# Performance work log

Measured on AMD Instinct MI355X. Metric: run time of the kernel, lower is better.

## Reference

```python
import jax, jax.numpy as jnp
import numpy as np

B, L, IN_DIM, OUT_DIM = 8, 128, 512, 512
DEP_NUM, DEP_DIM = 45, 16


def setup_inputs() -> dict:
    key = jax.random.key(0)
    ks = jax.random.split(key, 10)
    h = jax.random.normal(ks[0], (B, L, IN_DIM), dtype=jnp.float32)
    dep_type_matrix = jax.random.randint(ks[1], (B, L, L), 0, DEP_NUM, dtype=jnp.int32)
    aspect_mask = jnp.zeros((B, L), dtype=bool).at[:, 10:14].set(True)
    # params (torch Linear convention: y = x @ W.T + b); xavier-ish scale
    def xavier(k, shape):
        fan_in, fan_out = shape[1], shape[0]
        lim = jnp.sqrt(6.0 / (fan_in + fan_out))
        return jax.random.uniform(k, shape, jnp.float32, -lim, lim)
    emb = jax.random.normal(ks[2], (DEP_NUM, DEP_DIM), dtype=jnp.float32)
    W1 = xavier(ks[3], (OUT_DIM, IN_DIM + DEP_DIM))
    b1 = jnp.zeros((OUT_DIM,), jnp.float32)
    W2 = xavier(ks[4], (OUT_DIM, IN_DIM + DEP_DIM))
    b2 = jnp.zeros((OUT_DIM,), jnp.float32)
    Wg = xavier(ks[5], (OUT_DIM, IN_DIM))
    bg = jnp.zeros((OUT_DIM,), jnp.float32)
    bias = jnp.zeros((OUT_DIM,), jnp.float32)
    return {"h": h, "dep_type_matrix": dep_type_matrix, "aspect_mask": aspect_mask,
            "emb": emb, "W1": W1, "b1": b1, "W2": W2, "b2": b2,
            "Wg": Wg, "bg": bg, "bias": bias}


def _position_aware(h, aspect_mask):
    # h: [B,L,D], aspect_mask: [B,L] bool
    Lh = h.shape[1]
    m = aspect_mask.astype(jnp.int32)
    start = jnp.argmax(m, axis=1)                       # first True
    end = Lh - 1 - jnp.argmax(jnp.flip(m, axis=1), axis=1)  # last True
    pos = jnp.arange(Lh)[None, :]                        # [1,L]
    s = start[:, None]
    e = end[:, None]
    inv_L = 1.0 / Lh
    left_w = 1.0 - (s - pos).astype(h.dtype) * inv_L
    right_w = 1.0 - (pos - e).astype(h.dtype) * inv_L
    w = jnp.where(pos < s, left_w, jnp.where(pos > e, right_w, 0.0))
    w = jnp.where(aspect_mask, 0.0, w)                   # zero on aspect words
    return h * w[:, :, None]


def reference(h, dep_type_matrix, aspect_mask, emb, W1, b1, W2, b2, Wg, bg, bias):
    D = h.shape[-1]
    h = _position_aware(h, aspect_mask)
    dep_emb = emb[dep_type_matrix]                       # [B,L,L,E]
    # split concat-linear: W(concat[h_i, e_ij]) = h_i @ Wh.T + e_ij @ Wd.T + b
    W1h, W1d = W1[:, :D], W1[:, D:]
    W2h, W2d = W2[:, :D], W2[:, D:]
    hp_i = jnp.einsum('bid,od->bio', h, W1h)[:, :, None, :] \
        + jnp.einsum('bije,oe->bijo', dep_emb, W1d) + b1   # [B,L,L,O]
    hp_j = jnp.einsum('bid,od->bio', h, W2h)[:, :, None, :] \
        + jnp.einsum('bije,oe->bijo', dep_emb, W2d) + b2   # [B,L,L,O]
    scores = jnp.exp(jnp.sum(hp_i * hp_j, axis=-1))        # [B,L,L]
    adj = (dep_type_matrix != 0).astype(scores.dtype)
    masked = scores * adj
    A = masked / (jnp.sum(masked, axis=-1, keepdims=True) + 1e-6)
    h_trans = jnp.einsum('bid,od->bio', h, Wg) + bg        # [B,L,O]
    out = jnp.einsum('bij,bjo->bio', A, h_trans) + bias
    return jax.nn.relu(out)
```

## Files before the change

### kernel.cpp

```cpp
#include <hip/hip_runtime.h>
#include <hip/hip_bf16.h>
#include <math.h>

#define NBATCH 8
#define NL 128
#define IND 512
#define DEPN 45
#define DEPD 16
#define WCOLS 528
#define NP 1664
#define C_P1 0
#define C_P2 512
#define C_HT 1024
#define C_D1 1536
#define C_D2 1581
#define C_PAD 1626

typedef __attribute__((ext_vector_type(8))) short bf16x8;
typedef __attribute__((ext_vector_type(4))) float f32x4;

__device__ inline ushort f2bf(float x) {
    __hip_bfloat16 b = __float2bfloat16(x);
    return *reinterpret_cast<ushort*>(&b);
}
__device__ inline float bf2f(ushort u) {
    __hip_bfloat16 b;
    *reinterpret_cast<ushort*>(&b) = u;
    return __bfloat162float(b);
}

__device__ __forceinline__ void gl16(const ushort* g, ushort* l) {
    __builtin_amdgcn_global_load_lds(
        (const __attribute__((address_space(1))) unsigned int*)g,
        (__attribute__((address_space(3))) unsigned int*)l, 16, 0, 0);
}

__global__ __launch_bounds__(256) void k_prep(
    const float* __restrict__ h, const unsigned char* __restrict__ mask,
    const float* __restrict__ emb,
    const float* __restrict__ W1, const float* __restrict__ W2,
    const float* __restrict__ Wg,
    const float* __restrict__ b1, const float* __restrict__ b2,
    const float* __restrict__ bg,
    ushort* __restrict__ A_hi, ushort* __restrict__ A_lo,
    ushort* __restrict__ B_hi, ushort* __restrict__ B_lo,
    float* __restrict__ bias_ext) {
    int bid = blockIdx.x;
    int tid = threadIdx.x;

    if (bid < 64) {
        int rb = bid * 16;
        int b = rb >> 7;
        __shared__ int sflag, smin, smax;
        __shared__ float w16[16];
        if (tid == 0) { sflag = 0; smin = NL; smax = -1; }
        __syncthreads();
        const int* mi = (const int*)mask;
        if (tid < 128) {
            int v0 = mi[tid], v1 = mi[tid + 128];
            if ((unsigned)v0 > 1u || (unsigned)v1 > 1u) atomicOr(&sflag, 1);
        }
        __syncthreads();
        if (tid < 128) {
            int mval = sflag ? (int)mask[b * NL + tid] : mi[b * NL + tid];
            if (mval) { atomicMin(&smin, tid); atomicMax(&smax, tid); }
        }
        __syncthreads();
        if (tid < 16) {
            int any = (smax >= 0);
            int s = any ? smin : 0;
            int e = any ? smax : (NL - 1);
            int i = (rb & 127) + tid;
            const float invL = 1.0f / (float)NL;
            float w;
            if (i < s)      w = 1.0f - (float)(s - i) * invL;
            else if (i > e) w = 1.0f - (float)(i - e) * invL;
            else            w = 0.0f;
            int mval = sflag ? (int)mask[b * NL + i] : mi[b * NL + i];
            if (mval) w = 0.0f;
            w16[tid] = w;
        }
        __syncthreads();
        for (int idx = tid; idx < 16 * 128; idx += 256) {
            int r = idx >> 7, dc = (idx & 127) << 2;
            float4 hv = *(const float4*)&h[(size_t)(rb + r) * IND + dc];
            float wv = w16[r];
            hv.x *= wv; hv.y *= wv; hv.z *= wv; hv.w *= wv;
            ushort4 hi4, lo4;
            hi4.x = f2bf(hv.x); hi4.y = f2bf(hv.y); hi4.z = f2bf(hv.z); hi4.w = f2bf(hv.w);
            lo4.x = f2bf(hv.x - bf2f(hi4.x));
            lo4.y = f2bf(hv.y - bf2f(hi4.y));
            lo4.z = f2bf(hv.z - bf2f(hi4.z));
            lo4.w = f2bf(hv.w - bf2f(hi4.w));
            *(ushort4*)&A_hi[(size_t)(rb + r) * IND + dc] = hi4;
            *(ushort4*)&A_lo[(size_t)(rb + r) * IND + dc] = lo4;
        }
        if (bid == 0) {
            for (int i = tid; i < 512; i += 256) {
                bias_ext[C_P1 + i] = b1[i];
                bias_ext[C_P2 + i] = b2[i];
                bias_ext[C_HT + i] = bg[i];
            }
            if (tid < NP - C_PAD) bias_ext[C_PAD + tid] = 0.f;
        }
    } else if (bid < 160) {
        int nb = (bid - 64) * 16;
        for (int idx = tid; idx < 16 * 128; idx += 256) {
            int r = idx >> 7, dc = (idx & 127) << 2;
            int n = nb + r;
            const float* src;
            if (n < 512)       src = W1 + (size_t)n * WCOLS + dc;
            else if (n < 1024) src = W2 + (size_t)(n - 512) * WCOLS + dc;
            else               src = Wg + (size_t)(n - 1024) * IND + dc;
            float4 wv = *(const float4*)src;
            ushort4 hi4, lo4;
            hi4.x = f2bf(wv.x); hi4.y = f2bf(wv.y); hi4.z = f2bf(wv.z); hi4.w = f2bf(wv.w);
            lo4.x = f2bf(wv.x - bf2f(hi4.x));
            lo4.y = f2bf(wv.y - bf2f(hi4.y));
            lo4.z = f2bf(wv.z - bf2f(hi4.z));
            lo4.w = f2bf(wv.w - bf2f(hi4.w));
            *(ushort4*)&B_hi[(size_t)n * IND + dc] = hi4;
            *(ushort4*)&B_lo[(size_t)n * IND + dc] = lo4;
        }
    } else if (bid < 162) {
        int nb = 1626 + (bid - 160) * 19;
        ushort4 z4 = {0, 0, 0, 0};
        for (int idx = tid; idx < 19 * 128; idx += 256) {
            int r = idx >> 7, dc = (idx & 127) << 2;
            *(ushort4*)&B_hi[(size_t)(nb + r) * IND + dc] = z4;
            *(ushort4*)&B_lo[(size_t)(nb + r) * IND + dc] = z4;
        }
    } else {
        int zi = bid - 162;
        int t = zi % 45;
        int m = (zi / 45) & 1;
        int dq = zi / 90;
        __shared__ float es[DEPD];
        __shared__ float ys[512];
        __shared__ float y1s[512];
        __shared__ float part[256];
        if (tid < DEPD) es[tid] = emb[t * DEPD + tid];
        __syncthreads();
        const float* Wdep = (m == 0) ? W2 : W1;
        for (int o = tid; o < 512; o += 256) {
            float s = 0.f;
#pragma unroll
            for (int e = 0; e < DEPD; e++) s += es[e] * Wdep[o * WCOLS + IND + e];
            ys[o] = s;
        }
        if (m == 0 && dq == 0) {
            for (int o = tid; o < 512; o += 256) {
                float s = 0.f;
#pragma unroll
                for (int e = 0; e < DEPD; e++) s += es[e] * W1[o * WCOLS + IND + e];
                y1s[o] = s;
            }
        }
        __syncthreads();
        int dloc = tid & 127, half = tid >> 7;
        const float* Wsrc = (m == 0) ? W1 : W2;
        int d = dq * 128 + dloc;
        int obase = half * 256;
        float s = 0.f;
#pragma unroll 16
        for (int oo = 0; oo < 256; oo++)
            s += Wsrc[(size_t)(obase + oo) * WCOLS + d] * ys[obase + oo];
        part[tid] = s;
        __syncthreads();
        int row = ((m == 0) ? C_D1 : C_D2) + t;
        if (half == 0) {
            float tot = part[dloc] + part[128 + dloc];
            ushort hi = f2bf(tot);
            B_hi[(size_t)row * IND + d] = hi;
            B_lo[(size_t)row * IND + d] = f2bf(tot - bf2f(hi));
        }
        if (dq == 0 && tid < 64) {
            const float* bb = (m == 0) ? b1 : b2;
            float sb = 0.f;
#pragma unroll
            for (int k = 0; k < 8; k++) sb += bb[tid + k * 64] * ys[tid + k * 64];
            if (m == 0) {
#pragma unroll
                for (int k = 0; k < 8; k++) sb += y1s[tid + k * 64] * ys[tid + k * 64];
            }
            for (int off = 32; off; off >>= 1) sb += __shfl_down(sb, off, 64);
            if (tid == 0) bias_ext[row] = sb;
        }
    }
}

__global__ __launch_bounds__(128) void k3_gemm(
    const ushort* __restrict__ A_hi, const ushort* __restrict__ A_lo,
    const ushort* __restrict__ B_hi, const ushort* __restrict__ B_lo,
    const float* __restrict__ bias_ext, float* __restrict__ Pout,
    ushort* __restrict__ HTb) {
    int tid = threadIdx.x;
    int wid = tid >> 6, lane = tid & 63;
    int lrow = lane & 15;
    int mbase = blockIdx.x * 32;
    int nbase = blockIdx.y * 64;

    __shared__ ushort Ah[16 * 32 * 8];
    __shared__ ushort Al[16 * 32 * 8];
    __shared__ ushort Bh[16 * 64 * 8];
    __shared__ ushort Bl[16 * 64 * 8];

    const ushort* aSrcH = A_hi + (size_t)(mbase + (lane & 31)) * IND + ((lane >> 5) << 3);
    const ushort* aSrcL = A_lo + (size_t)(mbase + (lane & 31)) * IND + ((lane >> 5) << 3);
    const ushort* bSrcH = B_hi + (size_t)(nbase + lane) * IND;
    const ushort* bSrcL = B_lo + (size_t)(nbase + lane) * IND;

#define STAGE(C) { \
    int ck = (C) * 128; \
    if (wid == 0) { \
        _Pragma("unroll") \
        for (int i = 0; i < 8; i++) gl16(aSrcH + ck + (i << 4), &Ah[i << 9]); \
        _Pragma("unroll") \
        for (int i = 0; i < 8; i++) gl16(aSrcL + ck + (i << 4), &Al[i << 9]); \
        _Pragma("unroll") \
        for (int g = 0; g < 8; g++) gl16(bSrcH + ck + (g << 3), &Bh[g << 9]); \
    } else { \
        _Pragma("unroll") \
        for (int g = 8; g < 16; g++) gl16(bSrcH + ck + (g << 3), &Bh[g << 9]); \
        _Pragma("unroll") \
        for (int g = 0; g < 16; g++) gl16(bSrcL + ck + (g << 3), &Bl[g << 9]); \
    } }

    f32x4 acc00 = {0.f, 0.f, 0.f, 0.f};
    f32x4 acc01 = acc00, acc10 = acc00, acc11 = acc00;

    STAGE(0)
    for (int c = 0; c < 4; c++) {
        __syncthreads();
#pragma unroll
        for (int KS = 0; KS < 4; KS++) {
            int gl = (KS << 2) + (lane >> 4);
            int ga = ((gl << 5) + lrow) << 3;
            int gb = ((gl << 6) + (wid << 5) + lrow) << 3;
            bf16x8 a0h = *(const bf16x8*)&Ah[ga];
            bf16x8 a0l = *(const bf16x8*)&Al[ga];
            bf16x8 a1h = *(const bf16x8*)&Ah[ga + 128];
            bf16x8 a1l = *(const bf16x8*)&Al[ga + 128];
            bf16x8 b0h = *(const bf16x8*)&Bh[gb];
            bf16x8 b0l = *(const bf16x8*)&Bl[gb];
            bf16x8 b1h = *(const bf16x8*)&Bh[gb + 128];
            bf16x8 b1l = *(const bf16x8*)&Bl[gb + 128];
            acc00 = __builtin_amdgcn_mfma_f32_16x16x32_bf16(a0h, b0h, acc00, 0, 0, 0);
            acc00 = __builtin_amdgcn_mfma_f32_16x16x32_bf16(a0h, b0l, acc00, 0, 0, 0);
            acc00 = __builtin_amdgcn_mfma_f32_16x16x32_bf16(a0l, b0h, acc00, 0, 0, 0);
            acc01 = __builtin_amdgcn_mfma_f32_16x16x32_bf16(a0h, b1h, acc01, 0, 0, 0);
            acc01 = __builtin_amdgcn_mfma_f32_16x16x32_bf16(a0h, b1l, acc01, 0, 0, 0);
            acc01 = __builtin_amdgcn_mfma_f32_16x16x32_bf16(a0l, b1h, acc01, 0, 0, 0);
            acc10 = __builtin_amdgcn_mfma_f32_16x16x32_bf16(a1h, b0h, acc10, 0, 0, 0);
            acc10 = __builtin_amdgcn_mfma_f32_16x16x32_bf16(a1h, b0l, acc10, 0, 0, 0);
            acc10 = __builtin_amdgcn_mfma_f32_16x16x32_bf16(a1l, b0h, acc10, 0, 0, 0);
            acc11 = __builtin_amdgcn_mfma_f32_16x16x32_bf16(a1h, b1h, acc11, 0, 0, 0);
            acc11 = __builtin_amdgcn_mfma_f32_16x16x32_bf16(a1h, b1l, acc11, 0, 0, 0);
            acc11 = __builtin_amdgcn_mfma_f32_16x16x32_bf16(a1l, b1h, acc11, 0, 0, 0);
        }
        if (c < 3) {
            __syncthreads();
            STAGE(c + 1)
        }
    }
#undef STAGE

    int r0 = (lane >> 4) << 2;
    int colb = nbase + (wid << 5);
    int col0 = colb + lrow;
    int col1 = col0 + 16;
    float bv0 = bias_ext[col0];
    float bv1 = bias_ext[col1];

    if (colb >= C_HT && colb < C_HT + 512) {
        int o0 = col0 - C_HT, o1 = col1 - C_HT;
#pragma unroll
        for (int r = 0; r < 4; ++r) {
            int row0 = mbase + r0 + r;
            int row1 = row0 + 16;
            HTb[(size_t)row0 * 512 + o0] = f2bf(acc00[r] + bv0);
            HTb[(size_t)row0 * 512 + o1] = f2bf(acc01[r] + bv1);
            HTb[(size_t)row1 * 512 + o0] = f2bf(acc10[r] + bv0);
            HTb[(size_t)row1 * 512 + o1] = f2bf(acc11[r] + bv1);
        }
    } else {
#pragma unroll
        for (int r = 0; r < 4; ++r) {
            int row0 = mbase + r0 + r;
            int row1 = row0 + 16;
            Pout[(size_t)row0 * NP + col0] = acc00[r] + bv0;
            Pout[(size_t)row0 * NP + col1] = acc01[r] + bv1;
            Pout[(size_t)row1 * NP + col0] = acc10[r] + bv0;
            Pout[(size_t)row1 * NP + col1] = acc11[r] + bv1;
        }
    }
}

__global__ __launch_bounds__(128) void k5_out(
    const float* __restrict__ P, const int* __restrict__ dep,
    const ushort* __restrict__ HTb, const float* __restrict__ bias,
    float* __restrict__ out) {
    int row = blockIdx.x;
    int b = row >> 7;
    int tid = threadIdx.x;
    __shared__ float comb[DEPN];
    __shared__ float a[NL];
    __shared__ float red[2];
    __shared__ float sumv;

    const float* Prow = P + (size_t)row * NP;
    float4 p1 = *(const float4*)(Prow + C_P1 + tid * 4);
    float4 p2 = *(const float4*)(Prow + C_P2 + tid * 4);
    float lc = p1.x * p2.x + p1.y * p2.y + p1.z * p2.z + p1.w * p2.w;
    for (int off = 32; off; off >>= 1) lc += __shfl_down(lc, off, 64);
    if ((tid & 63) == 0) red[tid >> 6] = lc;
    if (tid < DEPN) comb[tid] = Prow[C_D1 + tid] + Prow[C_D2 + tid];
    __syncthreads();

    float c0 = red[0] + red[1];
    int tt = dep[(size_t)row * NL + tid];
    float sc = (tt != 0) ? expf(c0 + comb[tt]) : 0.f;
    a[tid] = sc;
    __syncthreads();
    if (tid < 64) {
        float v = a[tid] + a[tid + 64];
        for (int off = 32; off; off >>= 1) v += __shfl_down(v, off, 64);
        if (tid == 0) sumv = v;
    }
    __syncthreads();
    float inv = 1.0f / (sumv + 1e-6f);
    if (tid < NL) a[tid] *= inv;
    __syncthreads();

    const ushort* htb = HTb + (size_t)b * NL * 512 + tid * 4;
    float sx = 0.f, sy = 0.f, sz = 0.f, sw = 0.f;
#pragma unroll 8
    for (int j = 0; j < NL; j += 2) {
        float a0 = a[j], a1 = a[j + 1];
        ushort4 v0 = *(const ushort4*)(htb + (size_t)j * 512);
        ushort4 v1 = *(const ushort4*)(htb + (size_t)(j + 1) * 512);
        sx += a0 * bf2f(v0.x) + a1 * bf2f(v1.x);
        sy += a0 * bf2f(v0.y) + a1 * bf2f(v1.y);
        sz += a0 * bf2f(v0.z) + a1 * bf2f(v1.z);
        sw += a0 * bf2f(v0.w) + a1 * bf2f(v1.w);
    }
    float4 bv = *(const float4*)&bias[tid * 4];
    float4 o;
    o.x = fmaxf(sx + bv.x, 0.f);
    o.y = fmaxf(sy + bv.y, 0.f);
    o.z = fmaxf(sz + bv.z, 0.f);
    o.w = fmaxf(sw + bv.w, 0.f);
    *(float4*)&out[(size_t)row * 512 + tid * 4] = o;
}

extern "C" void kernel_launch(void* const* d_in, const int* in_sizes, int n_in,
                              void* d_out, int out_size, void* d_ws, size_t ws_size,
                              hipStream_t stream) {
    const float* h    = (const float*)d_in[0];
    const int* dep    = (const int*)d_in[1];
    const unsigned char* mask = (const unsigned char*)d_in[2];
    const float* emb  = (const float*)d_in[3];
    const float* W1   = (const float*)d_in[4];
    const float* b1   = (const float*)d_in[5];
    const float* W2   = (const float*)d_in[6];
    const float* b2   = (const float*)d_in[7];
    const float* Wg   = (const float*)d_in[8];
    const float* bg   = (const float*)d_in[9];
    const float* bias = (const float*)d_in[10];
    float* out = (float*)d_out;

    char* p = (char*)d_ws;
    ushort* A_hi = (ushort*)p;  p += (size_t)1024 * 512 * 2;
    ushort* A_lo = (ushort*)p;  p += (size_t)1024 * 512 * 2;
    ushort* B_hi = (ushort*)p;  p += (size_t)NP * 512 * 2;
    ushort* B_lo = (ushort*)p;  p += (size_t)NP * 512 * 2;
    ushort* HTb = (ushort*)p;   p += (size_t)1024 * 512 * 2;
    float* bias_ext = (float*)p; p += NP * 4;
    float* Pout = (float*)p;

    k_prep<<<522, 256, 0, stream>>>(h, mask, emb, W1, W2, Wg, b1, b2, bg,
                                    A_hi, A_lo, B_hi, B_lo, bias_ext);
    dim3 g3(32, 26);
    k3_gemm<<<g3, 128, 0, stream>>>(A_hi, A_lo, B_hi, B_lo, bias_ext, Pout, HTb);
    k5_out<<<NBATCH * NL, 128, 0, stream>>>(Pout, dep, HTb, bias, out);
}
```

Measured before the change: 55.93 us.

## Batch dep-weight precompute, enlarge GEMM tiles, process four rows per output block

The prep kernel now handles five dependency types per block for the folded W·Wdep rows, and bias terms move to separate small blocks, which cuts the block count from 522 to 324. The GEMM uses 64x64 tiles with four waves and a 64-wide K step, so each staged tile is reused across more outputs. The output kernel handles four query rows per block, so each HT load is shared across four rows, and it folds normalization into the epilogue. These changes aim to reduce redundant global loads and launch overhead, at the cost of fewer blocks and less parallelism.

```diff
diff --git a/kernel.cpp b/kernel.cpp
--- a/kernel.cpp
+++ b/kernel.cpp
@@ -130,51 +130,81 @@
             *(ushort4*)&B_hi[(size_t)(nb + r) * IND + dc] = z4;
             *(ushort4*)&B_lo[(size_t)(nb + r) * IND + dc] = z4;
         }
-    } else {
+    } else if (bid < 234) {
         int zi = bid - 162;
-        int t = zi % 45;
-        int m = (zi / 45) & 1;
-        int dq = zi / 90;
-        __shared__ float es[DEPD];
-        __shared__ float ys[512];
-        __shared__ float y1s[512];
-        __shared__ float part[256];
-        if (tid < DEPD) es[tid] = emb[t * DEPD + tid];
+        int m = zi / 36;
+        int rest = zi % 36;
+        int dq = rest / 9;
+        int tq = rest % 9;
+        int tb = tq * 5;
+        __shared__ float es5[5][DEPD];
+        __shared__ float ys5[5][512];
+        __shared__ float part[5][256];
+        if (tid < 5 * DEPD) es5[tid >> 4][tid & 15] = emb[(tb + (tid >> 4)) * DEPD + (tid & 15)];
         __syncthreads();
         const float* Wdep = (m == 0) ? W2 : W1;
-        for (int o = tid; o < 512; o += 256) {
+        for (int idx = tid; idx < 5 * 512; idx += 256) {
+            int tt = idx >> 9, o = idx & 511;
             float s = 0.f;
 #pragma unroll
-            for (int e = 0; e < DEPD; e++) s += es[e] * Wdep[o * WCOLS + IND + e];
-            ys[o] = s;
-        }
-        if (m == 0 && dq == 0) {
-            for (int o = tid; o < 512; o += 256) {
-                float s = 0.f;
-#pragma unroll
-                for (int e = 0; e < DEPD; e++) s += es[e] * W1[o * WCOLS + IND + e];
-                y1s[o] = s;
-            }
+            for (int e = 0; e < DEPD; e++) s += es5[tt][e] * Wdep[o * WCOLS + IND + e];
+            ys5[tt][o] = s;
         }
         __syncthreads();
         int dloc = tid & 127, half = tid >> 7;
         const float* Wsrc = (m == 0) ? W1 : W2;
         int d = dq * 128 + dloc;
         int obase = half * 256;
-        float s = 0.f;
-#pragma unroll 16
-        for (int oo = 0; oo < 256; oo++)
-            s += Wsrc[(size_t)(obase + oo) * WCOLS + d] * ys[obase + oo];
-        part[tid] = s;
-        __syncthreads();
-        int row = ((m == 0) ? C_D1 : C_D2) + t;
+        float ac0 = 0.f, ac1 = 0.f, ac2 = 0.f, ac3 = 0.f, ac4 = 0.f;
+#pragma unroll 8
+        for (int oo = 0; oo < 256; oo++) {
+            float w = Wsrc[(size_t)(obase + oo) * WCOLS + d];
+            int o = obase + oo;
+            ac0 += w * ys5[0][o];
+            ac1 += w * ys5[1][o];
+            ac2 += w * ys5[2][o];
+            ac3 += w * ys5[3][o];
+            ac4 += w * ys5[4][o];
+        }
+        part[0][tid] = ac0; part[1][tid] = ac1; part[2][tid] = ac2;
+        part[3][tid] = ac3; part[4][tid] = ac4;
+        __syncthreads();
         if (half == 0) {
-            float tot = part[dloc] + part[128 + dloc];
-            ushort hi = f2bf(tot);
-            B_hi[(size_t)row * IND + d] = hi;
-            B_lo[(size_t)row * IND + d] = f2bf(tot - bf2f(hi));
-        }
-        if (dq == 0 && tid < 64) {
+#pragma unroll
+            for (int tt = 0; tt < 5; tt++) {
+                float tot = part[tt][dloc] + part[tt][128 + dloc];
+                int row = ((m == 0) ? C_D1 : C_D2) + tb + tt;
+                ushort hi = f2bf(tot);
+                B_hi[(size_t)row * IND + d] = hi;
+                B_lo[(size_t)row * IND + d] = f2bf(tot - bf2f(hi));
+            }
+        }
+    } else {
+        int zi2 = bid - 234;
+        int t = zi2 % 45;
+        int m = zi2 / 45;
+        __shared__ float es[DEPD];
+        __shared__ float ys[512];
+        __shared__ float y1s[512];
+        if (tid < DEPD) es[tid] = emb[t * DEPD + tid];
+        __syncthreads();
+        const float* Wdep = (m == 0) ? W2 : W1;
+        for (int o = tid; o < 512; o += 256) {
+            float s = 0.f;
+#pragma unroll
+            for (int e = 0; e < DEPD; e++) s += es[e] * Wdep[o * WCOLS + IND + e];
+            ys[o] = s;
+        }
+        if (m == 0) {
+            for (int o = tid; o < 512; o += 256) {
+                float s = 0.f;
+#pragma unroll
+                for (int e = 0; e < DEPD; e++) s += es[e] * W1[o * WCOLS + IND + e];
+                y1s[o] = s;
+            }
+        }
+        __syncthreads();
+        if (tid < 64) {
             const float* bb = (m == 0) ? b1 : b2;
             float sb = 0.f;
 #pragma unroll
@@ -184,12 +214,12 @@
                 for (int k = 0; k < 8; k++) sb += y1s[tid + k * 64] * ys[tid + k * 64];
             }
             for (int off = 32; off; off >>= 1) sb += __shfl_down(sb, off, 64);
-            if (tid == 0) bias_ext[row] = sb;
-        }
-    }
-}
-
-__global__ __launch_bounds__(128) void k3_gemm(
+            if (tid == 0) bias_ext[((m == 0) ? C_D1 : C_D2) + t] = sb;
+        }
+    }
+}
+
+__global__ __launch_bounds__(256) void k3_gemm(
     const ushort* __restrict__ A_hi, const ushort* __restrict__ A_lo,
     const ushort* __restrict__ B_hi, const ushort* __restrict__ B_lo,
     const float* __restrict__ bias_ext, float* __restrict__ Pout,
@@ -197,46 +227,48 @@
     int tid = threadIdx.x;
     int wid = tid >> 6, lane = tid & 63;
     int lrow = lane & 15;
-    int mbase = blockIdx.x * 32;
+    int mbase = blockIdx.x * 64;
     int nbase = blockIdx.y * 64;
-
-    __shared__ ushort Ah[16 * 32 * 8];
-    __shared__ ushort Al[16 * 32 * 8];
-    __shared__ ushort Bh[16 * 64 * 8];
-    __shared__ ushort Bl[16 * 64 * 8];
-
-    const ushort* aSrcH = A_hi + (size_t)(mbase + (lane & 31)) * IND + ((lane >> 5) << 3);
-    const ushort* aSrcL = A_lo + (size_t)(mbase + (lane & 31)) * IND + ((lane >> 5) << 3);
-    const ushort* bSrcH = B_hi + (size_t)(nbase + lane) * IND;
-    const ushort* bSrcL = B_lo + (size_t)(nbase + lane) * IND;
+    int mh = (wid >> 1) << 5;
+    int nh = (wid & 1) << 5;
+
+    __shared__ ushort Ah[8 * 64 * 8];
+    __shared__ ushort Al[8 * 64 * 8];
+    __shared__ ushort Bh[8 * 64 * 8];
+    __shared__ ushort Bl[8 * 64 * 8];
+
+    const ushort* aH = A_hi + (size_t)(mbase + lane) * IND;
+    const ushort* aL = A_lo + (size_t)(mbase + lane) * IND;
+    const ushort* bH = B_hi + (size_t)(nbase + lane) * IND;
+    const ushort* bL = B_lo + (size_t)(nbase + lane) * IND;
 
 #define STAGE(C) { \
-    int ck = (C) * 128; \
+    int ck = (C) << 6; \
     if (wid == 0) { \
         _Pragma("unroll") \
-        for (int i = 0; i < 8; i++) gl16(aSrcH + ck + (i << 4), &Ah[i << 9]); \
+        for (int g = 0; g < 8; g++) gl16(aH + ck + (g << 3), &Ah[g << 9]); \
+    } else if (wid == 1) { \
         _Pragma("unroll") \
-        for (int i = 0; i < 8; i++) gl16(aSrcL + ck + (i << 4), &Al[i << 9]); \
+        for (int g = 0; g < 8; g++) gl16(aL + ck + (g << 3), &Al[g << 9]); \
+    } else if (wid == 2) { \
         _Pragma("unroll") \
-        for (int g = 0; g < 8; g++) gl16(bSrcH + ck + (g << 3), &Bh[g << 9]); \
+        for (int g = 0; g < 8; g++) gl16(bH + ck + (g << 3), &Bh[g << 9]); \
     } else { \
         _Pragma("unroll") \
-        for (int g = 8; g < 16; g++) gl16(bSrcH + ck + (g << 3), &Bh[g << 9]); \
-        _Pragma("unroll") \
-        for (int g = 0; g < 16; g++) gl16(bSrcL + ck + (g << 3), &Bl[g << 9]); \
+        for (int g = 0; g < 8; g++) gl16(bL + ck + (g << 3), &Bl[g << 9]); \
     } }
 
     f32x4 acc00 = {0.f, 0.f, 0.f, 0.f};
     f32x4 acc01 = acc00, acc10 = acc00, acc11 = acc00;
 
     STAGE(0)
-    for (int c = 0; c < 4; c++) {
-        __syncthreads();
-#pragma unroll
-        for (int KS = 0; KS < 4; KS++) {
-            int gl = (KS << 2) + (lane >> 4);
-            int ga = ((gl << 5) + lrow) << 3;
-            int gb = ((gl << 6) + (wid << 5) + lrow) << 3;
+    for (int c = 0; c < 8; c++) {
+        __syncthreads();
+#pragma unroll
+        for (int KS = 0; KS < 2; KS++) {
+            int gA = (KS << 2) + (lane >> 4);
+            int ga = ((gA << 6) + mh + lrow) << 3;
+            int gb = ((gA << 6) + nh + lrow) << 3;
             bf16x8 a0h = *(const bf16x8*)&Ah[ga];
             bf16x8 a0l = *(const bf16x8*)&Al[ga];
             bf16x8 a1h = *(const bf16x8*)&Ah[ga + 128];
@@ -258,7 +290,7 @@
             acc11 = __builtin_amdgcn_mfma_f32_16x16x32_bf16(a1h, b1l, acc11, 0, 0, 0);
             acc11 = __builtin_amdgcn_mfma_f32_16x16x32_bf16(a1l, b1h, acc11, 0, 0, 0);
         }
-        if (c < 3) {
+        if (c < 7) {
             __syncthreads();
             STAGE(c + 1)
         }
@@ -266,17 +298,18 @@
 #undef STAGE
 
     int r0 = (lane >> 4) << 2;
-    int colb = nbase + (wid << 5);
+    int colb = nbase + nh;
     int col0 = colb + lrow;
     int col1 = col0 + 16;
     float bv0 = bias_ext[col0];
     float bv1 = bias_ext[col1];
+    int rowb = mbase + mh;
 
     if (colb >= C_HT && colb < C_HT + 512) {
         int o0 = col0 - C_HT, o1 = col1 - C_HT;
 #pragma unroll
         for (int r = 0; r < 4; ++r) {
-            int row0 = mbase + r0 + r;
+            int row0 = rowb + r0 + r;
             int row1 = row0 + 16;
             HTb[(size_t)row0 * 512 + o0] = f2bf(acc00[r] + bv0);
             HTb[(size_t)row0 * 512 + o1] = f2bf(acc01[r] + bv1);
@@ -286,7 +319,7 @@
     } else {
 #pragma unroll
         for (int r = 0; r < 4; ++r) {
-            int row0 = mbase + r0 + r;
+            int row0 = rowb + r0 + r;
             int row1 = row0 + 16;
             Pout[(size_t)row0 * NP + col0] = acc00[r] + bv0;
             Pout[(size_t)row0 * NP + col1] = acc01[r] + bv1;
@@ -296,61 +329,79 @@
     }
 }
 
-__global__ __launch_bounds__(128) void k5_out(
+__global__ __launch_bounds__(256) void k5_out(
     const float* __restrict__ P, const int* __restrict__ dep,
     const ushort* __restrict__ HTb, const float* __restrict__ bias,
     float* __restrict__ out) {
-    int row = blockIdx.x;
-    int b = row >> 7;
+    int blk = blockIdx.x;
+    int b = blk >> 5;
+    int i0 = b * 128 + (blk & 31) * 4;
     int tid = threadIdx.x;
-    __shared__ float comb[DEPN];
-    __shared__ float a[NL];
-    __shared__ float red[2];
-    __shared__ float sumv;
-
-    const float* Prow = P + (size_t)row * NP;
-    float4 p1 = *(const float4*)(Prow + C_P1 + tid * 4);
-    float4 p2 = *(const float4*)(Prow + C_P2 + tid * 4);
-    float lc = p1.x * p2.x + p1.y * p2.y + p1.z * p2.z + p1.w * p2.w;
-    for (int off = 32; off; off >>= 1) lc += __shfl_down(lc, off, 64);
-    if ((tid & 63) == 0) red[tid >> 6] = lc;
-    if (tid < DEPN) comb[tid] = Prow[C_D1 + tid] + Prow[C_D2 + tid];
+    int wr = tid >> 6, lane = tid & 63;
+    __shared__ float a[4][NL];
+    __shared__ float c0s[4];
+    __shared__ float comb[4][48];
+    __shared__ float invs[4];
+
+    {
+        const float* p1 = P + (size_t)(i0 + wr) * NP + C_P1 + lane * 8;
+        const float* p2 = P + (size_t)(i0 + wr) * NP + C_P2 + lane * 8;
+        float4 x0 = *(const float4*)(p1);
+        float4 x1 = *(const float4*)(p1 + 4);
+        float4 y0 = *(const float4*)(p2);
+        float4 y1 = *(const float4*)(p2 + 4);
+        float s = x0.x * y0.x + x0.y * y0.y + x0.z * y0.z + x0.w * y0.w
+                + x1.x * y1.x + x1.y * y1.y + x1.z * y1.z + x1.w * y1.w;
+        for (int off = 32; off; off >>= 1) s += __shfl_down(s, off, 64);
+        if (lane == 0) c0s[wr] = s;
+    }
+    for (int idx = tid; idx < 4 * 45; idx += 256) {
+        int r = idx / 45, t = idx - r * 45;
+        const float* Prow = P + (size_t)(i0 + r) * NP;
+        comb[r][t] = Prow[C_D1 + t] + Prow[C_D2 + t];
+    }
     __syncthreads();
 
-    float c0 = red[0] + red[1];
-    int tt = dep[(size_t)row * NL + tid];
-    float sc = (tt != 0) ? expf(c0 + comb[tt]) : 0.f;
-    a[tid] = sc;
+#pragma unroll
+    for (int k = 0; k < 2; k++) {
+        int idx = tid + k * 256;
+        int r = idx >> 7, j = idx & 127;
+        int tt = dep[(size_t)(i0 + r) * NL + j];
+        a[r][j] = (tt != 0) ? expf(c0s[r] + comb[r][tt]) : 0.f;
+    }
     __syncthreads();
-    if (tid < 64) {
-        float v = a[tid] + a[tid + 64];
+    {
+        float v = a[wr][lane] + a[wr][lane + 64];
         for (int off = 32; off; off >>= 1) v += __shfl_down(v, off, 64);
-        if (tid == 0) sumv = v;
+        if (lane == 0) invs[wr] = 1.0f / (v + 1e-6f);
     }
     __syncthreads();
-    float inv = 1.0f / (sumv + 1e-6f);
-    if (tid < NL) a[tid] *= inv;
-    __syncthreads();
-
-    const ushort* htb = HTb + (size_t)b * NL * 512 + tid * 4;
-    float sx = 0.f, sy = 0.f, sz = 0.f, sw = 0.f;
+
+    int o2 = tid * 2;
+    float s00 = 0.f, s01 = 0.f, s10 = 0.f, s11 = 0.f;
+    float s20 = 0.f, s21 = 0.f, s30 = 0.f, s31 = 0.f;
+    const ushort* hp = HTb + (size_t)b * NL * 512 + o2;
 #pragma unroll 8
-    for (int j = 0; j < NL; j += 2) {
-        float a0 = a[j], a1 = a[j + 1];
-        ushort4 v0 = *(const ushort4*)(htb + (size_t)j * 512);
-        ushort4 v1 = *(const ushort4*)(htb + (size_t)(j + 1) * 512);
-        sx += a0 * bf2f(v0.x) + a1 * bf2f(v1.x);
-        sy += a0 * bf2f(v0.y) + a1 * bf2f(v1.y);
-        sz += a0 * bf2f(v0.z) + a1 * bf2f(v1.z);
-        sw += a0 * bf2f(v0.w) + a1 * bf2f(v1.w);
-    }
-    float4 bv = *(const float4*)&bias[tid * 4];
-    float4 o;
-    o.x = fmaxf(sx + bv.x, 0.f);
-    o.y = fmaxf(sy + bv.y, 0.f);
-    o.z = fmaxf(sz + bv.z, 0.f);
-    o.w = fmaxf(sw + bv.w, 0.f);
-    *(float4*)&out[(size_t)row * 512 + tid * 4] = o;
+    for (int j = 0; j < NL; j++) {
+        ushort2 hv = *(const ushort2*)(hp + (size_t)j * 512);
+        float h0 = bf2f(hv.x), h1 = bf2f(hv.y);
+        float a0 = a[0][j], a1 = a[1][j], a2 = a[2][j], a3 = a[3][j];
+        s00 += a0 * h0; s01 += a0 * h1;
+        s10 += a1 * h0; s11 += a1 * h1;
+        s20 += a2 * h0; s21 += a2 * h1;
+        s30 += a3 * h0; s31 += a3 * h1;
+    }
+    float bv0 = bias[o2], bv1 = bias[o2 + 1];
+    float i0v = invs[0], i1v = invs[1], i2v = invs[2], i3v = invs[3];
+    float2 o;
+    o.x = fmaxf(s00 * i0v + bv0, 0.f); o.y = fmaxf(s01 * i0v + bv1, 0.f);
+    *(float2*)&out[(size_t)(i0 + 0) * 512 + o2] = o;
+    o.x = fmaxf(s10 * i1v + bv0, 0.f); o.y = fmaxf(s11 * i1v + bv1, 0.f);
+    *(float2*)&out[(size_t)(i0 + 1) * 512 + o2] = o;
+    o.x = fmaxf(s20 * i2v + bv0, 0.f); o.y = fmaxf(s21 * i2v + bv1, 0.f);
+    *(float2*)&out[(size_t)(i0 + 2) * 512 + o2] = o;
+    o.x = fmaxf(s30 * i3v + bv0, 0.f); o.y = fmaxf(s31 * i3v + bv1, 0.f);
+    *(float2*)&out[(size_t)(i0 + 3) * 512 + o2] = o;
 }
 
 extern "C" void kernel_launch(void* const* d_in, const int* in_sizes, int n_in,
@@ -378,9 +429,9 @@
     float* bias_ext = (float*)p; p += NP * 4;
     float* Pout = (float*)p;
 
-    k_prep<<<522, 256, 0, stream>>>(h, mask, emb, W1, W2, Wg, b1, b2, bg,
+    k_prep<<<324, 256, 0, stream>>>(h, mask, emb, W1, W2, Wg, b1, b2, bg,
                                     A_hi, A_lo, B_hi, B_lo, bias_ext);
-    dim3 g3(32, 26);
-    k3_gemm<<<g3, 128, 0, stream>>>(A_hi, A_lo, B_hi, B_lo, bias_ext, Pout, HTb);
-    k5_out<<<NBATCH * NL, 128, 0, stream>>>(Pout, dep, HTb, bias, out);
-}
+    dim3 g3(16, 26);
+    k3_gemm<<<g3, 256, 0, stream>>>(A_hi, A_lo, B_hi, B_lo, bias_ext, Pout, HTb);
+    k5_out<<<256, 256, 0, stream>>>(Pout, dep, HTb, bias, out);
+}
```

New measurement: 54.64 us. -2.3%, faster.
